# Optimization experiments

Hardware: AMD Instinct MI355X
Metric: run time of the kernel (lower is better)

The kernel has to match this reference:

```python
import jax, jax.numpy as jnp
import numpy as np
from jax import lax

DN = ('NCHW', 'OIHW', 'NCHW')

def _conv(x, w, b, stride, pad):
    o = lax.conv_general_dilated(x, w, (stride, stride), [(pad, pad), (pad, pad)], dimension_numbers=DN)
    return o + b[None, :, None, None]

def _conv_transpose(x, w, b, stride, pad):
    # w in torch ConvTranspose2d layout [Cin, Cout, kh, kw]
    k = w.shape[2]
    wf = jnp.flip(w, (2, 3)).transpose(1, 0, 2, 3)  # -> [Cout, Cin, kh, kw]
    p = k - 1 - pad
    o = lax.conv_general_dilated(x, wf, (1, 1), [(p, p), (p, p)], lhs_dilation=(stride, stride), dimension_numbers=DN)
    return o + b[None, :, None, None]

def setup_inputs() -> dict:
    key = jax.random.key(0)
    ks = jax.random.split(key, 16)
    s = 0.05
    NUM_EMB, EMB_DIM = 512, 128
    inp = {
        'x': jax.random.normal(ks[0], (32, 1, 224, 224), jnp.float32),
        # encoder
        'w_e1': jax.random.normal(ks[1], (64, 1, 4, 4), jnp.float32) * s,
        'b_e1': jnp.zeros((64,), jnp.float32),
        'w_e2': jax.random.normal(ks[2], (128, 64, 4, 4), jnp.float32) * s,
        'b_e2': jnp.zeros((128,), jnp.float32),
        'w_e3': jax.random.normal(ks[3], (128, 128, 3, 3), jnp.float32) * s,
        'b_e3': jnp.zeros((128,), jnp.float32),
        # codebook (torch init: uniform(-1/K, 1/K))
        'emb': jax.random.uniform(ks[4], (NUM_EMB, EMB_DIM), jnp.float32, -1.0 / NUM_EMB, 1.0 / NUM_EMB),
        # decoder
        'w_d1': jax.random.normal(ks[5], (128, 128, 3, 3), jnp.float32) * s,
        'b_d1': jnp.zeros((128,), jnp.float32),
        'w_dt1': jax.random.normal(ks[6], (128, 64, 4, 4), jnp.float32) * s,  # ConvTranspose [Cin,Cout,k,k]
        'b_dt1': jnp.zeros((64,), jnp.float32),
        'w_dt2': jax.random.normal(ks[7], (64, 1, 4, 4), jnp.float32) * s,
        'b_dt2': jnp.zeros((1,), jnp.float32),
    }
    return inp

def reference(x, w_e1, b_e1, w_e2, b_e2, w_e3, b_e3, emb, w_d1, b_d1, w_dt1, b_dt1, w_dt2, b_dt2):
    sg = lax.stop_gradient
    # --- encoder ---
    h = jax.nn.relu(_conv(x, w_e1, b_e1, 2, 1))
    h = jax.nn.relu(_conv(h, w_e2, b_e2, 2, 1))
    z_e = _conv(h, w_e3, b_e3, 1, 1)  # [B,128,H/4,W/4]
    B, C, H, W = z_e.shape
    # --- vector quantizer (faithful to source, incl. missing -2*z@e.T cross term) ---
    z_flat = z_e.transpose(0, 2, 3, 1).reshape(-1, C)  # [BHW, C]
    distances = (z_flat ** 2).sum(1, keepdims=True) + (emb ** 2).sum(1)  # [BHW, K]
    indices = jnp.argmin(distances, axis=1)
    z_q = emb[indices].reshape(B, H, W, C).transpose(0, 3, 1, 2)
    codebook_loss = jnp.mean((z_q - sg(z_e)) ** 2)
    commitment_loss = jnp.mean((sg(z_q) - z_e) ** 2)
    vq_loss = codebook_loss + commitment_loss
    # --- decoder ---
    d = _conv(z_q, w_d1, b_d1, 1, 1)
    d = jax.nn.relu(_conv_transpose(d, w_dt1, b_dt1, 2, 1))
    reconstructed_x = _conv_transpose(d, w_dt2, b_dt2, 2, 1)
    reconstruction_loss = jnp.mean((reconstructed_x - x) ** 2)
    total_loss = reconstruction_loss + vq_loss
    return (reconstructed_x, total_loss, reconstruction_loss, vq_loss)
```

## Files before the change

### kernel.cpp

```cpp
#include <hip/hip_runtime.h>
#include <hip/hip_bf16.h>

using bf16 = __hip_bfloat16;
using short8 = __attribute__((ext_vector_type(8))) short;
using f32x16 = __attribute__((ext_vector_type(16))) float;

__device__ __forceinline__ ushort f2us(float v) {
    bf16 h = __float2bfloat16(v);
    return *reinterpret_cast<ushort*>(&h);
}

#define MFMA32(a, b, c) __builtin_amdgcn_mfma_f32_32x32x16_bf16((a), (b), (c), 0, 0, 0)

__device__ __forceinline__ void gload16(const void* g, void* l) {
    __builtin_amdgcn_global_load_lds(
        (const __attribute__((address_space(1))) unsigned int*)g,
        (__attribute__((address_space(3))) unsigned int*)l, 16, 0, 0);
}

__device__ __forceinline__ int cls8(int i) {
    if (i == 0) return 0;
    if (i == 1) return 1;
    if (i == 2) return 2;
    if (i == 109) return 5;
    if (i == 110) return 6;
    if (i == 111) return 7;
    return (i & 1) ? 4 : 3;
}

__global__ void k_codebook(const float* __restrict__ emb, float* __restrict__ c) {
    __shared__ float sval[512];
    __shared__ int   sidx[512];
    int k = threadIdx.x;
    float s = 0.f;
    const float4* e4 = (const float4*)(emb + k * 128);
    #pragma unroll
    for (int d = 0; d < 32; ++d) {
        float4 v = e4[d];
        s += v.x * v.x + v.y * v.y + v.z * v.z + v.w * v.w;
    }
    sval[k] = s; sidx[k] = k;
    __syncthreads();
    for (int off = 256; off > 0; off >>= 1) {
        if (k < off) {
            float v2 = sval[k + off]; int i2 = sidx[k + off];
            if (v2 < sval[k] || (v2 == sval[k] && i2 < sidx[k])) { sval[k] = v2; sidx[k] = i2; }
        }
        __syncthreads();
    }
    int kmin = sidx[0];
    if (k < 128) c[k] = emb[kmin * 128 + k];
}

__global__ __launch_bounds__(256) void k_prepack(const float* __restrict__ w_e2,
                                                 const float* __restrict__ w_e3,
                                                 ushort* __restrict__ Wb2f,
                                                 ushort* __restrict__ Wb3f) {
    int i = blockIdx.x * 256 + threadIdx.x;
    const int n2 = 131072;
    const int n3 = 147456;
    if (i < n2) {
        int j = i & 7, l = (i >> 3) & 63, ks = (i >> 9) & 3, mf = (i >> 11) & 1,
            mh = (i >> 12) & 1, tap = i >> 13;
        int co = mh * 64 + mf * 32 + (l & 31);
        int ci = ks * 16 + (l >> 5) * 8 + j;
        int kh = tap >> 2, kw = tap & 3;
        Wb2f[i] = f2us(w_e2[((co * 64 + ci) * 4 + kh) * 4 + kw]);
    } else if (i < n2 + n3) {
        int t = i - n2;
        int j = t & 7, l = (t >> 3) & 63, ks = (t >> 9) & 7, mf = (t >> 12) & 1,
            mh = (t >> 13) & 1, tap = t >> 14;
        int co = mh * 64 + mf * 32 + (l & 31);
        int ci = ks * 16 + (l >> 5) * 8 + j;
        int kh = tap / 3, kw = tap % 3;
        Wb3f[t] = f2us(w_e3[((co * 128 + ci) * 3 + kh) * 3 + kw]);
    }
}

__global__ __launch_bounds__(256) void k_conv1(const float* __restrict__ x,
                                               const float* __restrict__ w,
                                               const float* __restrict__ bias,
                                               ushort* __restrict__ h1s) {
    __shared__ float wl[1024];
    __shared__ float bl[64];
    __shared__ __align__(16) char obuf[28672];
    int tid = threadIdx.x;
    for (int i = tid; i < 1024; i += 256) wl[i] = w[i];
    if (tid < 64) bl[tid] = bias[tid];
    __syncthreads();
    int r = blockIdx.x, b = blockIdx.y;
    int g = tid >> 6;
    int q = tid & 63;
    bool act = q < 56;
    int oh = 2 * r + (q >= 28);
    int ow0 = (q % 28) * 4;

    float xv[4][10];
    const float* xb = x + (size_t)b * 50176;
    #pragma unroll
    for (int kh = 0; kh < 4; ++kh) {
        int ih = 2 * oh - 1 + kh;
        bool rok = act && (unsigned)ih < 224u;
        #pragma unroll
        for (int j = 0; j < 10; ++j) {
            int iw = 2 * ow0 - 1 + j;
            xv[kh][j] = (rok && (unsigned)iw < 224u) ? xb[ih * 224 + iw] : 0.f;
        }
    }
    float a[4][16];
    #pragma unroll
    for (int i = 0; i < 4; ++i)
        #pragma unroll
        for (int j = 0; j < 16; ++j) a[i][j] = 0.f;

    const float4* wl4 = (const float4*)wl;
    #pragma unroll
    for (int j = 0; j < 16; ++j) {
        int co = g * 16 + j;
        #pragma unroll
        for (int kh = 0; kh < 4; ++kh) {
            float4 wr = wl4[co * 4 + kh];
            #pragma unroll
            for (int i = 0; i < 4; ++i) {
                a[i][j] += xv[kh][2*i+0]*wr.x + xv[kh][2*i+1]*wr.y
                         + xv[kh][2*i+2]*wr.z + xv[kh][2*i+3]*wr.w;
            }
        }
    }
    if (act) {
        #pragma unroll
        for (int i = 0; i < 4; ++i) {
            int ow = ow0 + i, wq = ow >> 1, pw = ow & 1;
            char* rowb = obuf + (oh & 1) * 14336 + wq * 256;
            int key = (wq & 15) << 4;
            #pragma unroll
            for (int j = 0; j < 16; ++j) {
                int co = g * 16 + j;
                *(ushort*)(rowb + ((pw * 128 + co * 2) ^ key)) =
                    f2us(fmaxf(a[i][j] + bl[co], 0.f));
            }
        }
    }
    __syncthreads();
    const float4* sb = (const float4*)obuf;
    for (int i = tid; i < 1792; i += 256) {
        int ph = (i >= 896) ? 1 : 0;
        float4* dst = (float4*)((char*)h1s + (((size_t)(b * 2 + ph)) * 56 + r) * 14336);
        dst[i - ph * 896] = sb[i];
    }
}

__global__ __launch_bounds__(256, 1) void k_conv2_mfma(const ushort* __restrict__ h1s,
                                                       const ushort* __restrict__ Wb2f,
                                                       const float* __restrict__ bias,
                                                       ushort* __restrict__ h2s) {
    __shared__ __align__(16) char ldsc[6 * 14848];
    int lin = blockIdx.x;
    int v = (lin & 7) * 112 + (lin >> 3);
    int b = v / 28, ohp = v % 28, oh0 = ohp * 2;
    int tid = threadIdx.x, lane = tid & 63, wv = tid >> 6;
    int mh = wv & 1, r = wv >> 1;
    int lrow = lane & 31, khalf = lane >> 5;
    const float4 z4 = {0.f, 0.f, 0.f, 0.f};

    if (tid < 192) {
        int s = tid >> 5, rr = (tid >> 4) & 1, col = tid & 15;
        ((float4*)(ldsc + s * 14848 + rr * 57 * 256))[col] = z4;
    }
    #pragma unroll
    for (int s = 0; s < 6; ++s) {
        int ph = (s < 3) ? 0 : 1;
        int rr = (s < 3) ? (oh0 + s) : (oh0 - 4 + s);
        char* ldst = ldsc + s * 14848 + 256;
        if ((unsigned)rr < 56u) {
            const char* src = (const char*)h1s + (((size_t)(b * 2 + ph)) * 56 + rr) * 14336;
            for (int c2 = wv; c2 < 14; c2 += 4)
                gload16(src + c2 * 1024 + lane * 16, ldst + c2 * 1024);
        } else {
            for (int i = tid; i < 896; i += 256) ((float4*)ldst)[i] = z4;
        }
    }
    __syncthreads();

    const f32x16 vz = {0,0,0,0,0,0,0,0,0,0,0,0,0,0,0,0};
    f32x16 acc[2][2];
    #pragma unroll
    for (int cf = 0; cf < 2; ++cf)
        #pragma unroll
        for (int mf = 0; mf < 2; ++mf) acc[cf][mf] = vz;

    int slab_of[4] = {3 + r, r, 4 + r, 1 + r};
    #pragma unroll
    for (int kh = 0; kh < 4; ++kh) {
        const char* slab = ldsc + slab_of[kh] * 14848;
        #pragma unroll
        for (int kw = 0; kw < 4; ++kw) {
            int tap = kh * 4 + kw;
            int pw = (kw & 1) ? 0 : 1;
            int wofs = (kw == 0) ? 0 : (kw == 3) ? 2 : 1;
            const char* abase = (const char*)Wb2f +
                ((size_t)(tap * 2 + mh) * 2 * 4) * 1024 + lane * 16;
            short8 af[2][4];
            #pragma unroll
            for (int mf = 0; mf < 2; ++mf)
                #pragma unroll
                for (int ks = 0; ks < 4; ++ks)
                    af[mf][ks] = *(const short8*)(abase + (mf * 4 + ks) * 1024);
            int colb = pw * 128 + khalf * 16;
            #pragma unroll
            for (int cf = 0; cf < 2; ++cf) {
                int wp = cf * 24 + lrow + wofs;
                int key = ((wp - 1) & 15) << 4;
                const char* rowb = slab + wp * 256;
                #pragma unroll
                for (int ks = 0; ks < 4; ++ks) {
                    short8 bv = *(const short8*)(rowb + ((colb + ks * 32) ^ key));
                    acc[cf][0] = MFMA32(af[0][ks], bv, acc[cf][0]);
                    acc[cf][1] = MFMA32(af[1][ks], bv, acc[cf][1]);
                }
            }
        }
    }
    __syncthreads();
    {
        char* obuf = ldsc + r * 14336;
        #pragma unroll
        for (int cf = 0; cf < 2; ++cf) {
            int ow = cf * 24 + lrow;
            if (cf == 0 || lrow >= 8) {
                char* rowb = obuf + ow * 256;
                int key = (ow & 15) << 4;
                #pragma unroll
                for (int mf = 0; mf < 2; ++mf)
                    #pragma unroll
                    for (int reg = 0; reg < 16; ++reg) {
                        int co = mh * 64 + mf * 32 + (reg & 3) + 8 * (reg >> 2) + 4 * khalf;
                        float vv = fmaxf(acc[cf][mf][reg] + bias[co], 0.f);
                        *(ushort*)(rowb + ((co * 2) ^ key)) = f2us(vv);
                    }
            }
        }
    }
    __syncthreads();
    const float4* sb = (const float4*)ldsc;
    for (int i = tid; i < 1792; i += 256) {
        int rr = (i >= 896) ? 1 : 0;
        float4* dst = (float4*)((char*)h2s + ((size_t)(b * 56) + oh0 + rr) * 14336);
        dst[i - rr * 896] = sb[i];
    }
}

__global__ __launch_bounds__(128, 1) void k_conv3_mfma(const ushort* __restrict__ h2s,
                                                       const ushort* __restrict__ Wb3f,
                                                       const float* __restrict__ bias,
                                                       const float* __restrict__ c,
                                                       float* __restrict__ vq_part) {
    __shared__ __align__(16) char ldsc[4 * 14848];
    __shared__ float red[2];
    int lin = blockIdx.x;
    int v = (lin & 7) * 112 + (lin >> 3);
    int b = v / 28, ohp = v % 28, oh0 = ohp * 2;
    int tid = threadIdx.x, lane = tid & 63, mh = tid >> 6;
    int lrow = lane & 31, khalf = lane >> 5;
    const float4 z4 = {0.f, 0.f, 0.f, 0.f};

    {
        int s = tid >> 5, rr = (tid >> 4) & 1, col = tid & 15;
        ((float4*)(ldsc + s * 14848 + rr * 57 * 256))[col] = z4;
    }
    #pragma unroll
    for (int s = 0; s < 4; ++s) {
        int rr = oh0 - 1 + s;
        char* ldst = ldsc + s * 14848 + 256;
        if ((unsigned)rr < 56u) {
            const char* src = (const char*)h2s + ((size_t)b * 56 + rr) * 14336;
            for (int c2 = mh; c2 < 14; c2 += 2)
                gload16(src + c2 * 1024 + lane * 16, ldst + c2 * 1024);
        } else {
            for (int i = tid; i < 896; i += 128) ((float4*)ldst)[i] = z4;
        }
    }
    __syncthreads();

    const f32x16 vz = {0,0,0,0,0,0,0,0,0,0,0,0,0,0,0,0};
    f32x16 acc[2][2][2];
    #pragma unroll
    for (int r = 0; r < 2; ++r)
        #pragma unroll
        for (int cf = 0; cf < 2; ++cf)
            #pragma unroll
            for (int mf = 0; mf < 2; ++mf) acc[r][cf][mf] = vz;

    #pragma unroll
    for (int kh = 0; kh < 3; ++kh) {
        #pragma unroll
        for (int kw = 0; kw < 3; ++kw) {
            int tap = kh * 3 + kw;
            const char* abase = (const char*)Wb3f +
                ((size_t)(tap * 2 + mh) * 2 * 8) * 1024 + lane * 16;
            short8 af[2][8];
            #pragma unroll
            for (int mf = 0; mf < 2; ++mf)
                #pragma unroll
                for (int ks = 0; ks < 8; ++ks)
                    af[mf][ks] = *(const short8*)(abase + (mf * 8 + ks) * 1024);
            #pragma unroll
            for (int r = 0; r < 2; ++r) {
                const char* slab = ldsc + (r + kh) * 14848;
                #pragma unroll
                for (int cf = 0; cf < 2; ++cf) {
                    int wp = cf * 24 + lrow + kw;
                    int key = ((wp - 1) & 15) << 4;
                    const char* rowb = slab + wp * 256;
                    #pragma unroll
                    for (int ks = 0; ks < 8; ++ks) {
                        short8 bv = *(const short8*)(rowb + ((khalf * 16 + ks * 32) ^ key));
                        acc[r][cf][0] = MFMA32(af[0][ks], bv, acc[r][cf][0]);
                        acc[r][cf][1] = MFMA32(af[1][ks], bv, acc[r][cf][1]);
                    }
                }
            }
        }
    }
    float ls = 0.f;
    #pragma unroll
    for (int r = 0; r < 2; ++r)
        #pragma unroll
        for (int cf = 0; cf < 2; ++cf) {
            if (cf == 0 || lrow >= 8) {
                #pragma unroll
                for (int mf = 0; mf < 2; ++mf)
                    #pragma unroll
                    for (int reg = 0; reg < 16; ++reg) {
                        int co = mh * 64 + mf * 32 + (reg & 3) + 8 * (reg >> 2) + 4 * khalf;
                        float z = acc[r][cf][mf][reg] + bias[co];
                        float d = c[co] - z;
                        ls += d * d;
                    }
            }
        }
    #pragma unroll
    for (int off = 32; off > 0; off >>= 1) ls += __shfl_down(ls, off);
    if (lane == 0) red[mh] = ls;
    __syncthreads();
    if (tid == 0) vq_part[v] = red[0] + red[1];
}

__global__ __launch_bounds__(128) void k_SD3(const float* __restrict__ w_d1,
                                             const float* __restrict__ c,
                                             const float* __restrict__ b_d1,
                                             float* __restrict__ D3) {
    int co = blockIdx.x, ci = threadIdx.x;
    __shared__ float cl[128];
    __shared__ float part[9][128];
    cl[ci] = c[ci];
    __syncthreads();
    const float* wp = w_d1 + (co * 128 + ci) * 9;
    float cv = cl[ci];
    #pragma unroll
    for (int t = 0; t < 9; ++t) part[t][ci] = wp[t] * cv;
    __syncthreads();
    for (int off = 64; off > 0; off >>= 1) {
        if (ci < off) {
            #pragma unroll
            for (int t = 0; t < 9; ++t) part[t][ci] += part[t][ci + off];
        }
        __syncthreads();
    }
    if (ci < 9) {
        int rh = ci / 3, rw = ci % 3;
        int kh0 = (rh == 0) ? 1 : 0, kh1 = (rh == 2) ? 1 : 2;
        int kw0 = (rw == 0) ? 1 : 0, kw1 = (rw == 2) ? 1 : 2;
        float a = b_d1[co];
        for (int kh = kh0; kh <= kh1; ++kh)
            for (int kw = kw0; kw <= kw1; ++kw)
                a += part[kh * 3 + kw][0];
        D3[co * 9 + ci] = a;
    }
}

__global__ __launch_bounds__(64) void k_d2c(const float* __restrict__ D3,
                                            const float* __restrict__ w_dt1,
                                            const float* __restrict__ b_dt1,
                                            float* __restrict__ d2c) {
    __shared__ float dl[1152];
    int gh = blockIdx.x, gw = blockIdx.y, co2 = threadIdx.x;
    for (int i = co2; i < 1152; i += 64) dl[i] = D3[i];
    __syncthreads();
    const int rep[8] = {0, 1, 2, 4, 3, 109, 110, 111};
    int oh = rep[gh], ow = rep[gw];
    float a = b_dt1[co2];
    #pragma unroll
    for (int th = 0; th < 2; ++th) {
        int kh = ((oh + 1) & 1) + 2 * th;
        int ih = (oh + 1 - kh) >> 1;
        if ((unsigned)ih >= 56u) continue;
        int rh = (ih == 0) ? 0 : (ih == 55) ? 2 : 1;
        #pragma unroll
        for (int tw = 0; tw < 2; ++tw) {
            int kw = ((ow + 1) & 1) + 2 * tw;
            int iw = (ow + 1 - kw) >> 1;
            if ((unsigned)iw >= 56u) continue;
            int rw = (iw == 0) ? 0 : (iw == 55) ? 2 : 1;
            float t = 0.f;
            for (int ci = 0; ci < 128; ++ci)
                t += dl[ci * 9 + rh * 3 + rw] * w_dt1[(ci * 64 + co2) * 16 + kh * 4 + kw];
            a += t;
        }
    }
    d2c[(gh * 8 + gw) * 64 + co2] = fmaxf(a, 0.f);
}

__global__ __launch_bounds__(256) void k_Rbuild(const float* __restrict__ d2c,
                                                const float* __restrict__ w_dt2,
                                                const float* __restrict__ b_dt2,
                                                float* __restrict__ R) {
    __shared__ float el[1024];
    int tid = threadIdx.x;
    #pragma unroll
    for (int q = 0; q < 4; ++q) {
        int id = tid * 4 + q;
        int kh = id >> 8, kw = (id >> 6) & 3, gh = (id >> 3) & 7, gw = id & 7;
        float t = 0.f;
        const float* dp = d2c + (gh * 8 + gw) * 64;
        const float* wp = w_dt2 + kh * 4 + kw;
        for (int ci = 0; ci < 64; ++ci) t += dp[ci] * wp[ci * 16];
        el[((kh * 4 + kw) * 8 + gh) * 8 + gw] = t;
    }
    __syncthreads();
    int s = blockIdx.x * 256 + tid;
    int oh = s / 224, ow = s % 224;
    float a = b_dt2[0];
    #pragma unroll
    for (int th = 0; th < 2; ++th) {
        int kh = ((oh + 1) & 1) + 2 * th;
        int ih = (oh + 1 - kh) >> 1;
        if ((unsigned)ih >= 112u) continue;
        int ch = cls8(ih);
        #pragma unroll
        for (int tw = 0; tw < 2; ++tw) {
            int kw = ((ow + 1) & 1) + 2 * tw;
            int iw = (ow + 1 - kw) >> 1;
            if ((unsigned)iw >= 112u) continue;
            int cw = cls8(iw);
            a += el[((kh * 4 + kw) * 8 + ch) * 8 + cw];
        }
    }
    R[s] = a;
}

__global__ __launch_bounds__(256) void k_out(const float* __restrict__ R,
                                             const float* __restrict__ x,
                                             float* __restrict__ out,
                                             float* __restrict__ rec_part) {
    int i4 = blockIdx.x * 256 + threadIdx.x;
    int s4 = i4 % 12544;
    float4 r = ((const float4*)R)[s4];
    float4 xv = ((const float4*)x)[i4];
    ((float4*)out)[i4] = r;
    float dx = r.x - xv.x, dy = r.y - xv.y, dz = r.z - xv.z, dw = r.w - xv.w;
    float v = dx * dx + dy * dy + dz * dz + dw * dw;
    __shared__ float red[4];
    #pragma unroll
    for (int off = 32; off > 0; off >>= 1) v += __shfl_down(v, off);
    int wid = threadIdx.x >> 6, lane = threadIdx.x & 63;
    if (lane == 0) red[wid] = v;
    __syncthreads();
    if (threadIdx.x == 0) rec_part[blockIdx.x] = red[0] + red[1] + red[2] + red[3];
}

__global__ __launch_bounds__(256) void k_fin(const float* __restrict__ vq_part,
                                             const float* __restrict__ rec_part,
                                             float* __restrict__ out, int loss_base) {
    __shared__ float sv[256], sr[256];
    float a = 0.f, b2 = 0.f;
    for (int i = threadIdx.x; i < 896;  i += 256) a  += vq_part[i];
    for (int i = threadIdx.x; i < 1568; i += 256) b2 += rec_part[i];
    sv[threadIdx.x] = a; sr[threadIdx.x] = b2;
    __syncthreads();
    for (int off = 128; off > 0; off >>= 1) {
        if (threadIdx.x < off) { sv[threadIdx.x] += sv[threadIdx.x + off]; sr[threadIdx.x] += sr[threadIdx.x + off]; }
        __syncthreads();
    }
    if (threadIdx.x == 0) {
        float vq  = 2.f * sv[0] / 12845056.f;
        float rec = sr[0] / 1605632.f;
        out[loss_base + 0] = rec + vq;
        out[loss_base + 1] = rec;
        out[loss_base + 2] = vq;
    }
}

extern "C" void kernel_launch(void* const* d_in, const int* in_sizes, int n_in,
                              void* d_out, int out_size, void* d_ws, size_t ws_size,
                              hipStream_t stream) {
    const float* x     = (const float*)d_in[0];
    const float* w_e1  = (const float*)d_in[1];
    const float* b_e1  = (const float*)d_in[2];
    const float* w_e2  = (const float*)d_in[3];
    const float* b_e2  = (const float*)d_in[4];
    const float* w_e3  = (const float*)d_in[5];
    const float* b_e3  = (const float*)d_in[6];
    const float* emb   = (const float*)d_in[7];
    const float* w_d1  = (const float*)d_in[8];
    const float* b_d1  = (const float*)d_in[9];
    const float* w_dt1 = (const float*)d_in[10];
    const float* b_dt1 = (const float*)d_in[11];
    const float* w_dt2 = (const float*)d_in[12];
    const float* b_dt2 = (const float*)d_in[13];
    float* out = (float*)d_out;
    float* ws  = (float*)d_ws;

    float* c        = ws + 16;
    float* D3       = ws + 256;
    float* d2c      = ws + 2048;
    float* R        = ws + 8192;
    float* vq_part  = ws + 65536;
    float* rec_part = ws + 67584;
    ushort* Wb2f    = (ushort*)(ws + 131072);
    ushort* Wb3f    = (ushort*)(ws + 196608);
    ushort* h1s     = (ushort*)(ws + 1310720);
    ushort* h2s     = (ushort*)(ws + 14155776);

    k_codebook<<<1, 512, 0, stream>>>(emb, c);
    k_prepack<<<1088, 256, 0, stream>>>(w_e2, w_e3, Wb2f, Wb3f);
    k_conv1<<<dim3(56, 32), 256, 0, stream>>>(x, w_e1, b_e1, h1s);
    k_conv2_mfma<<<896, 256, 0, stream>>>(h1s, Wb2f, b_e2, h2s);
    k_conv3_mfma<<<896, 128, 0, stream>>>(h2s, Wb3f, b_e3, c, vq_part);
    k_SD3<<<128, 128, 0, stream>>>(w_d1, c, b_d1, D3);
    k_d2c<<<dim3(8, 8), 64, 0, stream>>>(D3, w_dt1, b_dt1, d2c);
    k_Rbuild<<<196, 256, 0, stream>>>(d2c, w_dt2, b_dt2, R);
    k_out<<<1568, 256, 0, stream>>>(R, x, out, rec_part);
    k_fin<<<1, 256, 0, stream>>>(vq_part, rec_part, out, out_size - 3);
}
```

Baseline: 192.8 us.

## Enlarge conv2/conv3 row tiles to 4 rows and double-buffer weight fragments

conv2 and conv3 blocks now compute four output rows with 512 threads, reusing loaded input halo rows across more outputs and halving the grid. Weight MFMA fragments are double-buffered in registers so the next tap's global loads overlap the current MFMAs. The output/loss kernel processes two vectors per thread with half the blocks. Larger LDS footprints (about 148KB for conv2) limit blocks per CU and may raise register pressure.

```diff
diff --git a/kernel.cpp b/kernel.cpp
--- a/kernel.cpp
+++ b/kernel.cpp
@@ -150,36 +150,48 @@
     }
 }
 
-__global__ __launch_bounds__(256, 1) void k_conv2_mfma(const ushort* __restrict__ h1s,
+#define LOADA2(buf, tp) { \
+    const char* ab_ = (const char*)Wb2f + ((size_t)(((tp) * 2 + mh) * 8)) * 1024 + lane * 16; \
+    _Pragma("unroll") \
+    for (int mf_ = 0; mf_ < 2; ++mf_) { \
+        _Pragma("unroll") \
+        for (int ks_ = 0; ks_ < 4; ++ks_) \
+            af[buf][mf_][ks_] = *(const short8*)(ab_ + (mf_ * 4 + ks_) * 1024); \
+    } }
+
+__global__ __launch_bounds__(512, 2) void k_conv2_mfma(const ushort* __restrict__ h1s,
                                                        const ushort* __restrict__ Wb2f,
                                                        const float* __restrict__ bias,
                                                        ushort* __restrict__ h2s) {
-    __shared__ __align__(16) char ldsc[6 * 14848];
+    __shared__ __align__(16) char ldsc[10 * 14848];
     int lin = blockIdx.x;
-    int v = (lin & 7) * 112 + (lin >> 3);
-    int b = v / 28, ohp = v % 28, oh0 = ohp * 2;
+    int v = (lin & 7) * 56 + (lin >> 3);
+    int b = v / 14, oh0 = (v % 14) * 4;
     int tid = threadIdx.x, lane = tid & 63, wv = tid >> 6;
     int mh = wv & 1, r = wv >> 1;
     int lrow = lane & 31, khalf = lane >> 5;
     const float4 z4 = {0.f, 0.f, 0.f, 0.f};
 
-    if (tid < 192) {
+    if (tid < 320) {
         int s = tid >> 5, rr = (tid >> 4) & 1, col = tid & 15;
         ((float4*)(ldsc + s * 14848 + rr * 57 * 256))[col] = z4;
     }
     #pragma unroll
-    for (int s = 0; s < 6; ++s) {
-        int ph = (s < 3) ? 0 : 1;
-        int rr = (s < 3) ? (oh0 + s) : (oh0 - 4 + s);
+    for (int s = 0; s < 10; ++s) {
+        int ph = (s < 5) ? 0 : 1;
+        int rr = (s < 5) ? (oh0 + s) : (oh0 - 6 + s);
         char* ldst = ldsc + s * 14848 + 256;
         if ((unsigned)rr < 56u) {
             const char* src = (const char*)h1s + (((size_t)(b * 2 + ph)) * 56 + rr) * 14336;
-            for (int c2 = wv; c2 < 14; c2 += 4)
+            for (int c2 = wv; c2 < 14; c2 += 8)
                 gload16(src + c2 * 1024 + lane * 16, ldst + c2 * 1024);
         } else {
-            for (int i = tid; i < 896; i += 256) ((float4*)ldst)[i] = z4;
-        }
-    }
+            for (int i = tid; i < 896; i += 512) ((float4*)ldst)[i] = z4;
+        }
+    }
+    short8 af[2][2][4];
+    LOADA2(0, 0)
+    LOADA2(1, 1)
     __syncthreads();
 
     const f32x16 vz = {0,0,0,0,0,0,0,0,0,0,0,0,0,0,0,0};
@@ -189,37 +201,28 @@
         #pragma unroll
         for (int mf = 0; mf < 2; ++mf) acc[cf][mf] = vz;
 
-    int slab_of[4] = {3 + r, r, 4 + r, 1 + r};
-    #pragma unroll
-    for (int kh = 0; kh < 4; ++kh) {
-        const char* slab = ldsc + slab_of[kh] * 14848;
-        #pragma unroll
-        for (int kw = 0; kw < 4; ++kw) {
-            int tap = kh * 4 + kw;
-            int pw = (kw & 1) ? 0 : 1;
-            int wofs = (kw == 0) ? 0 : (kw == 3) ? 2 : 1;
-            const char* abase = (const char*)Wb2f +
-                ((size_t)(tap * 2 + mh) * 2 * 4) * 1024 + lane * 16;
-            short8 af[2][4];
+    #pragma unroll
+    for (int tap = 0; tap < 16; ++tap) {
+        const int kh = tap >> 2, kw = tap & 3;
+        const int pw = (kw & 1) ? 0 : 1;
+        const int wofs = (kw == 0) ? 0 : (kw == 3) ? 2 : 1;
+        const int sbase = (kh == 0) ? 5 : (kh == 1) ? 0 : (kh == 2) ? 6 : 1;
+        const char* slab = ldsc + (sbase + r) * 14848;
+        const int colb = pw * 128 + khalf * 16;
+        const int cur = tap & 1;
+        #pragma unroll
+        for (int cf = 0; cf < 2; ++cf) {
+            int wp = cf * 24 + lrow + wofs;
+            int key = ((wp - 1) & 15) << 4;
+            const char* rowb = slab + wp * 256;
             #pragma unroll
-            for (int mf = 0; mf < 2; ++mf)
-                #pragma unroll
-                for (int ks = 0; ks < 4; ++ks)
-                    af[mf][ks] = *(const short8*)(abase + (mf * 4 + ks) * 1024);
-            int colb = pw * 128 + khalf * 16;
-            #pragma unroll
-            for (int cf = 0; cf < 2; ++cf) {
-                int wp = cf * 24 + lrow + wofs;
-                int key = ((wp - 1) & 15) << 4;
-                const char* rowb = slab + wp * 256;
-                #pragma unroll
-                for (int ks = 0; ks < 4; ++ks) {
-                    short8 bv = *(const short8*)(rowb + ((colb + ks * 32) ^ key));
-                    acc[cf][0] = MFMA32(af[0][ks], bv, acc[cf][0]);
-                    acc[cf][1] = MFMA32(af[1][ks], bv, acc[cf][1]);
-                }
+            for (int ks = 0; ks < 4; ++ks) {
+                short8 bv = *(const short8*)(rowb + ((colb + ks * 32) ^ key));
+                acc[cf][0] = MFMA32(af[cur][0][ks], bv, acc[cf][0]);
+                acc[cf][1] = MFMA32(af[cur][1][ks], bv, acc[cf][1]);
             }
         }
+        if (tap < 14) { LOADA2(cur, tap + 2) }
     }
     __syncthreads();
     {
@@ -243,107 +246,109 @@
     }
     __syncthreads();
     const float4* sb = (const float4*)ldsc;
-    for (int i = tid; i < 1792; i += 256) {
-        int rr = (i >= 896) ? 1 : 0;
+    for (int i = tid; i < 3584; i += 512) {
+        int rr = i / 896;
         float4* dst = (float4*)((char*)h2s + ((size_t)(b * 56) + oh0 + rr) * 14336);
         dst[i - rr * 896] = sb[i];
     }
 }
 
-__global__ __launch_bounds__(128, 1) void k_conv3_mfma(const ushort* __restrict__ h2s,
+#define LOADA3(buf, tp) { \
+    const char* ab_ = (const char*)Wb3f + ((size_t)(((tp) * 2 + mh) * 16)) * 1024 + lane * 16; \
+    _Pragma("unroll") \
+    for (int mf_ = 0; mf_ < 2; ++mf_) { \
+        _Pragma("unroll") \
+        for (int ks_ = 0; ks_ < 8; ++ks_) \
+            af[buf][mf_][ks_] = *(const short8*)(ab_ + (mf_ * 8 + ks_) * 1024); \
+    } }
+
+__global__ __launch_bounds__(512, 2) void k_conv3_mfma(const ushort* __restrict__ h2s,
                                                        const ushort* __restrict__ Wb3f,
                                                        const float* __restrict__ bias,
                                                        const float* __restrict__ c,
                                                        float* __restrict__ vq_part) {
-    __shared__ __align__(16) char ldsc[4 * 14848];
-    __shared__ float red[2];
+    __shared__ __align__(16) char ldsc[6 * 14848];
+    __shared__ float red[8];
     int lin = blockIdx.x;
-    int v = (lin & 7) * 112 + (lin >> 3);
-    int b = v / 28, ohp = v % 28, oh0 = ohp * 2;
-    int tid = threadIdx.x, lane = tid & 63, mh = tid >> 6;
+    int v = (lin & 7) * 56 + (lin >> 3);
+    int b = v / 14, oh0 = (v % 14) * 4;
+    int tid = threadIdx.x, lane = tid & 63, wv = tid >> 6;
+    int mh = wv & 1, r = wv >> 1;
     int lrow = lane & 31, khalf = lane >> 5;
     const float4 z4 = {0.f, 0.f, 0.f, 0.f};
 
-    {
+    if (tid < 192) {
         int s = tid >> 5, rr = (tid >> 4) & 1, col = tid & 15;
         ((float4*)(ldsc + s * 14848 + rr * 57 * 256))[col] = z4;
     }
     #pragma unroll
-    for (int s = 0; s < 4; ++s) {
+    for (int s = 0; s < 6; ++s) {
         int rr = oh0 - 1 + s;
         char* ldst = ldsc + s * 14848 + 256;
         if ((unsigned)rr < 56u) {
             const char* src = (const char*)h2s + ((size_t)b * 56 + rr) * 14336;
-            for (int c2 = mh; c2 < 14; c2 += 2)
+            for (int c2 = wv; c2 < 14; c2 += 8)
                 gload16(src + c2 * 1024 + lane * 16, ldst + c2 * 1024);
         } else {
-            for (int i = tid; i < 896; i += 128) ((float4*)ldst)[i] = z4;
-        }
-    }
+            for (int i = tid; i < 896; i += 512) ((float4*)ldst)[i] = z4;
+        }
+    }
+    short8 af[2][2][8];
+    LOADA3(0, 0)
+    LOADA3(1, 1)
     __syncthreads();
 
     const f32x16 vz = {0,0,0,0,0,0,0,0,0,0,0,0,0,0,0,0};
-    f32x16 acc[2][2][2];
-    #pragma unroll
-    for (int r = 0; r < 2; ++r)
-        #pragma unroll
-        for (int cf = 0; cf < 2; ++cf)
+    f32x16 acc[2][2];
+    #pragma unroll
+    for (int cf = 0; cf < 2; ++cf)
+        #pragma unroll
+        for (int mf = 0; mf < 2; ++mf) acc[cf][mf] = vz;
+
+    #pragma unroll
+    for (int tap = 0; tap < 9; ++tap) {
+        const int kh = tap / 3, kw = tap % 3;
+        const char* slab = ldsc + (r + kh) * 14848;
+        const int cur = tap & 1;
+        #pragma unroll
+        for (int cf = 0; cf < 2; ++cf) {
+            int wp = cf * 24 + lrow + kw;
+            int key = ((wp - 1) & 15) << 4;
+            const char* rowb = slab + wp * 256;
             #pragma unroll
-            for (int mf = 0; mf < 2; ++mf) acc[r][cf][mf] = vz;
-
-    #pragma unroll
-    for (int kh = 0; kh < 3; ++kh) {
-        #pragma unroll
-        for (int kw = 0; kw < 3; ++kw) {
-            int tap = kh * 3 + kw;
-            const char* abase = (const char*)Wb3f +
-                ((size_t)(tap * 2 + mh) * 2 * 8) * 1024 + lane * 16;
-            short8 af[2][8];
+            for (int ks = 0; ks < 8; ++ks) {
+                short8 bv = *(const short8*)(rowb + ((khalf * 16 + ks * 32) ^ key));
+                acc[cf][0] = MFMA32(af[cur][0][ks], bv, acc[cf][0]);
+                acc[cf][1] = MFMA32(af[cur][1][ks], bv, acc[cf][1]);
+            }
+        }
+        if (tap < 7) { LOADA3(cur, tap + 2) }
+    }
+    float ls = 0.f;
+    #pragma unroll
+    for (int cf = 0; cf < 2; ++cf) {
+        if (cf == 0 || lrow >= 8) {
             #pragma unroll
             for (int mf = 0; mf < 2; ++mf)
                 #pragma unroll
-                for (int ks = 0; ks < 8; ++ks)
-                    af[mf][ks] = *(const short8*)(abase + (mf * 8 + ks) * 1024);
-            #pragma unroll
-            for (int r = 0; r < 2; ++r) {
-                const char* slab = ldsc + (r + kh) * 14848;
-                #pragma unroll
-                for (int cf = 0; cf < 2; ++cf) {
-                    int wp = cf * 24 + lrow + kw;
-                    int key = ((wp - 1) & 15) << 4;
-                    const char* rowb = slab + wp * 256;
-                    #pragma unroll
-                    for (int ks = 0; ks < 8; ++ks) {
-                        short8 bv = *(const short8*)(rowb + ((khalf * 16 + ks * 32) ^ key));
-                        acc[r][cf][0] = MFMA32(af[0][ks], bv, acc[r][cf][0]);
-                        acc[r][cf][1] = MFMA32(af[1][ks], bv, acc[r][cf][1]);
-                    }
+                for (int reg = 0; reg < 16; ++reg) {
+                    int co = mh * 64 + mf * 32 + (reg & 3) + 8 * (reg >> 2) + 4 * khalf;
+                    float z = acc[cf][mf][reg] + bias[co];
+                    float d = c[co] - z;
+                    ls += d * d;
                 }
-            }
-        }
-    }
-    float ls = 0.f;
-    #pragma unroll
-    for (int r = 0; r < 2; ++r)
-        #pragma unroll
-        for (int cf = 0; cf < 2; ++cf) {
-            if (cf == 0 || lrow >= 8) {
-                #pragma unroll
-                for (int mf = 0; mf < 2; ++mf)
-                    #pragma unroll
-                    for (int reg = 0; reg < 16; ++reg) {
-                        int co = mh * 64 + mf * 32 + (reg & 3) + 8 * (reg >> 2) + 4 * khalf;
-                        float z = acc[r][cf][mf][reg] + bias[co];
-                        float d = c[co] - z;
-                        ls += d * d;
-                    }
-            }
-        }
+        }
+    }
     #pragma unroll
     for (int off = 32; off > 0; off >>= 1) ls += __shfl_down(ls, off);
-    if (lane == 0) red[mh] = ls;
-    __syncthreads();
-    if (tid == 0) vq_part[v] = red[0] + red[1];
+    if (lane == 0) red[wv] = ls;
+    __syncthreads();
+    if (tid == 0) {
+        float t = 0.f;
+        #pragma unroll
+        for (int i = 0; i < 8; ++i) t += red[i];
+        vq_part[v] = t;
+    }
 }
 
 __global__ __launch_bounds__(128) void k_SD3(const float* __restrict__ w_d1,
@@ -453,13 +458,18 @@
                                              const float* __restrict__ x,
                                              float* __restrict__ out,
                                              float* __restrict__ rec_part) {
-    int i4 = blockIdx.x * 256 + threadIdx.x;
-    int s4 = i4 % 12544;
-    float4 r = ((const float4*)R)[s4];
-    float4 xv = ((const float4*)x)[i4];
-    ((float4*)out)[i4] = r;
-    float dx = r.x - xv.x, dy = r.y - xv.y, dz = r.z - xv.z, dw = r.w - xv.w;
-    float v = dx * dx + dy * dy + dz * dz + dw * dw;
+    int base = blockIdx.x * 512 + threadIdx.x;
+    float v = 0.f;
+    #pragma unroll
+    for (int t = 0; t < 2; ++t) {
+        int i4 = base + t * 256;
+        int s4 = i4 % 12544;
+        float4 r = ((const float4*)R)[s4];
+        float4 xv = ((const float4*)x)[i4];
+        ((float4*)out)[i4] = r;
+        float dx = r.x - xv.x, dy = r.y - xv.y, dz = r.z - xv.z, dw = r.w - xv.w;
+        v += dx * dx + dy * dy + dz * dz + dw * dw;
+    }
     __shared__ float red[4];
     #pragma unroll
     for (int off = 32; off > 0; off >>= 1) v += __shfl_down(v, off);
@@ -474,8 +484,8 @@
                                              float* __restrict__ out, int loss_base) {
     __shared__ float sv[256], sr[256];
     float a = 0.f, b2 = 0.f;
-    for (int i = threadIdx.x; i < 896;  i += 256) a  += vq_part[i];
-    for (int i = threadIdx.x; i < 1568; i += 256) b2 += rec_part[i];
+    for (int i = threadIdx.x; i < 448; i += 256) a  += vq_part[i];
+    for (int i = threadIdx.x; i < 784; i += 256) b2 += rec_part[i];
     sv[threadIdx.x] = a; sr[threadIdx.x] = b2;
     __syncthreads();
     for (int off = 128; off > 0; off >>= 1) {
@@ -525,11 +535,11 @@
     k_codebook<<<1, 512, 0, stream>>>(emb, c);
     k_prepack<<<1088, 256, 0, stream>>>(w_e2, w_e3, Wb2f, Wb3f);
     k_conv1<<<dim3(56, 32), 256, 0, stream>>>(x, w_e1, b_e1, h1s);
-    k_conv2_mfma<<<896, 256, 0, stream>>>(h1s, Wb2f, b_e2, h2s);
-    k_conv3_mfma<<<896, 128, 0, stream>>>(h2s, Wb3f, b_e3, c, vq_part);
+    k_conv2_mfma<<<448, 512, 0, stream>>>(h1s, Wb2f, b_e2, h2s);
+    k_conv3_mfma<<<448, 512, 0, stream>>>(h2s, Wb3f, b_e3, c, vq_part);
     k_SD3<<<128, 128, 0, stream>>>(w_d1, c, b_d1, D3);
     k_d2c<<<dim3(8, 8), 64, 0, stream>>>(D3, w_dt1, b_dt1, d2c);
     k_Rbuild<<<196, 256, 0, stream>>>(d2c, w_dt2, b_dt2, R);
-    k_out<<<1568, 256, 0, stream>>>(R, x, out, rec_part);
+    k_out<<<784, 256, 0, stream>>>(R, x, out, rec_part);
     k_fin<<<1, 256, 0, stream>>>(vq_part, rec_part, out, out_size - 3);
 }
```

After: 200.9 us. 1.04x slower.
